# Optimization experiments

Measured on AMD Instinct MI355X. Metric: run time of the kernel, lower is better.

## Reference

```python
import jax, jax.numpy as jnp
import numpy as np

B, S, T = 256, 2048, 64


def setup_inputs() -> dict:
    key = jax.random.key(0)
    k1, k2, k3, k4, k5 = jax.random.split(key, 5)
    emissions = jax.random.normal(k1, (B, S, T), dtype=jnp.float32)
    tags = jax.random.randint(k2, (B, S), 0, T)
    mask = jnp.ones((B, S), dtype=jnp.int32)
    start_transitions = jax.random.uniform(k3, (T,), minval=-1.0, maxval=1.0, dtype=jnp.float32)
    end_transitions = jax.random.uniform(k4, (T,), minval=-1.0, maxval=1.0, dtype=jnp.float32)
    transitions = jax.random.uniform(k5, (T, T), minval=-1.0, maxval=1.0, dtype=jnp.float32)
    return {
        'emissions': emissions,
        'start_transitions': start_transitions,
        'end_transitions': end_transitions,
        'transitions': transitions,
        'tags': tags,
        'mask': mask,
    }


def _crf_nll(emissions, start_transitions, end_transitions, transitions, tags, mask):
    # batch_first=True -> convert to time-major like the torch code
    em = jnp.swapaxes(emissions, 0, 1)            # (S, B, T)
    tg = tags.T                                   # (S, B)
    mk = mask.T.astype(emissions.dtype)           # (S, B)
    barange = jnp.arange(em.shape[1])

    # ---- numerator: score of the gold tag path ----
    score0 = start_transitions[tg[0]] + em[0, barange, tg[0]]  # (B,)

    def num_step(score, inp):
        em_i, tg_prev, tg_i, m_i = inp
        score = score + (transitions[tg_prev, tg_i] + em_i[barange, tg_i]) * m_i
        return score, None

    numerator, _ = jax.lax.scan(num_step, score0, (em[1:], tg[:-1], tg[1:], mk[1:]))
    seq_ends = mk.sum(axis=0).astype(jnp.int32) - 1            # (B,)
    last_tags = tg[seq_ends, barange]
    numerator = numerator + end_transitions[last_tags]

    # ---- denominator: log partition via forward algorithm (log-sum-exp semiring) ----
    alpha0 = start_transitions + em[0]                          # (B, T)

    def den_step(alpha, inp):
        em_i, m_i = inp
        # (B, T_prev, T_next) broadcast-add, reduce over T_prev
        nxt = jax.nn.logsumexp(alpha[:, :, None] + transitions[None, :, :] + em_i[:, None, :], axis=1)
        alpha = jnp.where(m_i[:, None] > 0, nxt, alpha)
        return alpha, None

    alpha, _ = jax.lax.scan(den_step, alpha0, (em[1:], mk[1:]))
    denominator = jax.nn.logsumexp(alpha + end_transitions, axis=1)  # (B,)

    return -(numerator - denominator).mean()


def reference(emissions, start_transitions, end_transitions, transitions, tags, mask):
    return _crf_nll(emissions, start_transitions, end_transitions, transitions, tags, mask)
```

## Files before the change

kernel.cpp:

```cpp
#include <hip/hip_runtime.h>

#define BB 256
#define SS 2048
#define TT 64
#define KC 64
#define LC 32
#define WARM 48
#define NSTEP (WARM + LC)
#define DEN_WAVES (BB * 4)
#define NSLOT 128
#define SLOT_STRIDE 32
#define LN2 0.69314718055994531f
#define LOG2E 1.4426950408889634f

typedef __fp16 half2v __attribute__((ext_vector_type(2)));
typedef __fp16 half8v __attribute__((ext_vector_type(8)));
typedef float float4v __attribute__((ext_vector_type(4)));

__device__ __forceinline__ float4v mfma16(half8v a, half8v b, float4v c) {
  return __builtin_amdgcn_mfma_f32_16x16x32_f16(a, b, c, 0, 0, 0);
}

__global__ __launch_bounds__(64, 1) void crf_kernel(
    const float* __restrict__ em, const float* __restrict__ startT,
    const float* __restrict__ endT, const float* __restrict__ trans,
    const int* __restrict__ tags, const int* __restrict__ mask,
    float* __restrict__ acc, int slotmask) {
  const int lane = threadIdx.x;

  if (blockIdx.x >= DEN_WAVES) {
    const int bb = blockIdx.x - DEN_WAVES;
    const int* tg = tags + bb * SS;
    const int* mp = mask + bb * SS;
    const float* emb = em + (size_t)bb * SS * TT;
    float part = 0.f;
    int cnt = 0;
#pragma unroll 4
    for (int k = 0; k < SS / 64; ++k) {
      int i = k * 64 + lane;
      int m = mp[i];
      cnt += m;
      if (i >= 1 && m) {
        int t1 = tg[i], t0 = tg[i - 1];
        part += trans[t0 * TT + t1] + emb[(size_t)i * TT + t1];
      }
    }
#pragma unroll
    for (int o = 32; o > 0; o >>= 1) {
      part += __shfl_xor(part, o, 64);
      cnt += __shfl_xor(cnt, o, 64);
    }
    if (lane == 0) {
      int t0 = tg[0];
      float num = part + startT[t0] + emb[t0] + endT[tg[cnt - 1]];
      atomicAdd(acc + (size_t)(blockIdx.x & slotmask) * SLOT_STRIDE,
                -num * (1.0f / BB));
    }
    return;
  }

  const int w = blockIdx.x;
  const int L = (w & 7) * (DEN_WAVES / 8) + (w >> 3);
  const int bb = L >> 2;
  const int s = lane & 15;
  const int g = lane >> 4;
  const int c = (L & 3) * 16 + s;
  const float* emB = em + (size_t)bb * SS * TT;
  const size_t rowb = (size_t)bb * SS;

  half8v A[4][2];
#pragma unroll
  for (int mt = 0; mt < 4; ++mt)
#pragma unroll
    for (int kt = 0; kt < 2; ++kt) {
      half8v f;
#pragma unroll
      for (int e = 0; e < 8; e += 2) {
        int k0 = 32 * kt + 16 * (e >> 2) + 4 * g + (e & 3);
        int m = 16 * mt + s;
        float v0 = __expf(trans[k0 * TT + m]) * 0.03125f;
        float v1 = __expf(trans[(k0 + 1) * TT + m]) * 0.03125f;
        half2v p = __builtin_amdgcn_cvt_pkrtz(v0, v1);
        f[e] = p[0];
        f[e + 1] = p[1];
      }
      A[mt][kt] = f;
    }

  half8v B0, B1;
#pragma unroll
  for (int e = 0; e < 8; ++e) {
    B0[e] = (__fp16)0.015625f;
    B1[e] = (__fp16)0.015625f;
  }
  float v_ready = 0.015625f;
  int esum = 0, nsteps = 0;
  float sS = 0.f, gamma = 0.f;
  float4v tf0, tf1, tf2, tf3;

  const int base = c * LC - WARM + 1;

  float4v buf[4][4];

  auto PF = [&](int slot, int idx) {
    int p = base + idx;
    p = p < 0 ? 0 : (p > SS - 1 ? SS - 1 : p);
    const float* r = emB + (size_t)p * TT + 4 * g;
    __builtin_amdgcn_sched_barrier(0);
#pragma unroll
    for (int mt = 0; mt < 4; ++mt) buf[slot][mt] = *(const float4v*)(r + 16 * mt);
    __builtin_amdgcn_sched_barrier(0);
  };
  auto CORE = [&](const float4v (&x)[4]) {
    int eb = __builtin_bit_cast(int, v_ready) & 0x7f800000;
    float sc = __builtin_bit_cast(float, 0x7C000000 - eb);
    esum += eb >> 23;
    nsteps += 1;
    float4v xs0 = x[0] * sc, xs1 = x[1] * sc, xs2 = x[2] * sc, xs3 = x[3] * sc;
    const float4v z = {0.f, 0.f, 0.f, 0.f};
    tf0 = mfma16(A[0][0], B0, z);
    tf0 = mfma16(A[0][1], B1, tf0);
    tf1 = mfma16(A[1][0], B0, z);
    tf1 = mfma16(A[1][1], B1, tf1);
    tf2 = mfma16(A[2][0], B0, z);
    tf2 = mfma16(A[2][1], B1, tf2);
    tf3 = mfma16(A[3][0], B0, z);
    tf3 = mfma16(A[3][1], B1, tf3);
    tf0 *= xs0; tf1 *= xs1; tf2 *= xs2; tf3 *= xs3;
    v_ready = __shfl(tf0[0], s, 64);
    half2v p;
    p = __builtin_amdgcn_cvt_pkrtz(tf0[0], tf0[1]); B0[0] = p[0]; B0[1] = p[1];
    p = __builtin_amdgcn_cvt_pkrtz(tf0[2], tf0[3]); B0[2] = p[0]; B0[3] = p[1];
    p = __builtin_amdgcn_cvt_pkrtz(tf1[0], tf1[1]); B0[4] = p[0]; B0[5] = p[1];
    p = __builtin_amdgcn_cvt_pkrtz(tf1[2], tf1[3]); B0[6] = p[0]; B0[7] = p[1];
    p = __builtin_amdgcn_cvt_pkrtz(tf2[0], tf2[1]); B1[0] = p[0]; B1[1] = p[1];
    p = __builtin_amdgcn_cvt_pkrtz(tf2[2], tf2[3]); B1[2] = p[0]; B1[3] = p[1];
    p = __builtin_amdgcn_cvt_pkrtz(tf3[0], tf3[1]); B1[4] = p[0]; B1[5] = p[1];
    p = __builtin_amdgcn_cvt_pkrtz(tf3[2], tf3[3]); B1[6] = p[0]; B1[7] = p[1];
  };
  auto STEP = [&](int slot, int pfIdx, bool doPf) {
    float4v x[4];
#pragma unroll
    for (int mt = 0; mt < 4; ++mt)
#pragma unroll
      for (int e = 0; e < 4; ++e) x[mt][e] = __expf(buf[slot][mt][e]);
    if (doPf) PF(slot, pfIdx);
    CORE(x);
  };

#pragma unroll
  for (int k = 0; k < 4; ++k) PF(k, k);

  for (int idx = 0; idx < WARM; idx += 4) {
#pragma unroll
    for (int k = 0; k < 4; ++k) STEP(k, idx + k + 4, true);
  }

  {
    float q0b = v_ready;
    sS = __log2f(q0b) + (float)(6 + esum - 116 * nsteps);
    if (c == 0) {
      float aref = startT[0] + emB[0];
      gamma = aref * LOG2E;
      sS = 0.f;
      esum = 0;
      nsteps = 0;
      v_ready = 0.015625f;
#pragma unroll
      for (int e = 0; e < 8; ++e) {
        int t0i = 16 * (e >> 2) + 4 * g + (e & 3);
        B0[e] = (__fp16)(__expf(startT[t0i] + emB[t0i] - aref) * 0.015625f);
        B1[e] = (__fp16)(__expf(startT[t0i + 32] + emB[t0i + 32] - aref) *
                         0.015625f);
      }
    }
  }

  for (int idx = WARM; idx < NSTEP - 4; idx += 4) {
#pragma unroll
    for (int k = 0; k < 4; ++k) STEP(k, idx + k + 4, true);
  }
  STEP(0, 0, false);
  STEP(1, 0, false);
  STEP(2, 0, false);
  float qf;
  {
    half8v oB0 = B0, oB1 = B1;
    float4v o0 = tf0, o1 = tf1, o2 = tf2, o3 = tf3;
    int oes = esum, on = nsteps;
    float ov = v_ready;
    STEP(3, 0, false);
    int p = base + (NSTEP - 1);
    int pc = p > SS - 1 ? SS - 1 : p;
    bool act = (p >= 1) && (p <= SS - 1) && (mask[rowb + pc] != 0);
    qf = act ? v_ready : ov;
    if (!act) {
      B0 = oB0; B1 = oB1; esum = oes; nsteps = on;
      tf0 = o0; tf1 = o1; tf2 = o2; tf3 = o3;
    }
  }

  float eS = __log2f(qf) + (float)(6 + esum - 116 * nsteps) + gamma;
  float contrib = LN2 * (eS - sS);

  {
    float q0l = __log2f(qf);
    float4v ar0, ar1, ar2, ar3;
    float mx = -1e30f;
#pragma unroll
    for (int r = 0; r < 4; ++r) {
      ar0[r] = LN2 * (__log2f(tf0[r]) - q0l) + endT[4 * g + r];
      ar1[r] = LN2 * (__log2f(tf1[r]) - q0l) + endT[16 + 4 * g + r];
      ar2[r] = LN2 * (__log2f(tf2[r]) - q0l) + endT[32 + 4 * g + r];
      ar3[r] = LN2 * (__log2f(tf3[r]) - q0l) + endT[48 + 4 * g + r];
      mx = fmaxf(mx, fmaxf(fmaxf(ar0[r], ar1[r]), fmaxf(ar2[r], ar3[r])));
    }
    mx = fmaxf(mx, __shfl_xor(mx, 16, 64));
    mx = fmaxf(mx, __shfl_xor(mx, 32, 64));
    float ex = 0.f;
#pragma unroll
    for (int r = 0; r < 4; ++r)
      ex += __expf(ar0[r] - mx) + __expf(ar1[r] - mx) + __expf(ar2[r] - mx) +
            __expf(ar3[r] - mx);
    ex += __shfl_xor(ex, 16, 64);
    ex += __shfl_xor(ex, 32, 64);
    if (c == KC - 1) contrib += mx + __logf(ex);
  }

  float val = (g == 0) ? contrib : 0.f;
#pragma unroll
  for (int o = 32; o > 0; o >>= 1) val += __shfl_xor(val, o, 64);
  if (lane == 0)
    atomicAdd(acc + (size_t)(blockIdx.x & slotmask) * SLOT_STRIDE,
              val * (1.0f / BB));
}

__global__ __launch_bounds__(64) void reduce_kernel(const float* __restrict__ ws,
                                                    float* __restrict__ out) {
  float v = ws[(size_t)threadIdx.x * SLOT_STRIDE] +
            ws[(size_t)(threadIdx.x + 64) * SLOT_STRIDE];
#pragma unroll
  for (int o = 32; o > 0; o >>= 1) v += __shfl_xor(v, o, 64);
  if (threadIdx.x == 0) *out = v;
}

extern "C" void kernel_launch(void* const* d_in, const int* in_sizes, int n_in,
                              void* d_out, int out_size, void* d_ws, size_t ws_size,
                              hipStream_t stream) {
  const float* em = (const float*)d_in[0];
  const float* startT = (const float*)d_in[1];
  const float* endT = (const float*)d_in[2];
  const float* trans = (const float*)d_in[3];
  const int* tags = (const int*)d_in[4];
  const int* mask = (const int*)d_in[5];
  float* out = (float*)d_out;

  const size_t need = (size_t)NSLOT * SLOT_STRIDE * sizeof(float);
  if (d_ws && ws_size >= need) {
    (void)hipMemsetAsync(d_ws, 0, need, stream);
    crf_kernel<<<DEN_WAVES + BB, 64, 0, stream>>>(em, startT, endT, trans, tags,
                                                  mask, (float*)d_ws, NSLOT - 1);
    reduce_kernel<<<1, 64, 0, stream>>>((const float*)d_ws, out);
  } else {
    (void)hipMemsetAsync(out, 0, sizeof(float), stream);
    crf_kernel<<<DEN_WAVES + BB, 64, 0, stream>>>(em, startT, endT, trans, tags,
                                                  mask, out, 0);
  }
}
```

Measured before the change: 250.7 us.

## Stream emissions via global_load_lds into an 8-deep LDS ring, shorten warmup

Replaces the 4-slot register prefetch buffer with an 8-slot LDS ring filled by direct global-to-LDS loads, using explicit vmcnt waits to keep several steps of emission rows in flight. This is meant to hide global memory latency in the serial forward recurrence and to free registers. Warmup length also drops from 48 to 32 steps, so each chunk does less redundant work, at the risk of weaker convergence of the warmup approximation. The hand-written vmcnt counts depend on exactly four loads per slot, and the LDS reads rely on no other outstanding memory ops being counted.

```diff
diff --git a/kernel.cpp b/kernel.cpp
--- a/kernel.cpp
+++ b/kernel.cpp
@@ -5,8 +5,9 @@
 #define TT 64
 #define KC 64
 #define LC 32
-#define WARM 48
+#define WARM 32
 #define NSTEP (WARM + LC)
+#define DEPTH 8
 #define DEN_WAVES (BB * 4)
 #define NSLOT 128
 #define SLOT_STRIDE 32
@@ -21,11 +22,14 @@
   return __builtin_amdgcn_mfma_f32_16x16x32_f16(a, b, c, 0, 0, 0);
 }
 
+#define VMW(N) asm volatile("s_waitcnt vmcnt(" #N ")" ::: "memory")
+
 __global__ __launch_bounds__(64, 1) void crf_kernel(
     const float* __restrict__ em, const float* __restrict__ startT,
     const float* __restrict__ endT, const float* __restrict__ trans,
     const int* __restrict__ tags, const int* __restrict__ mask,
     float* __restrict__ acc, int slotmask) {
+  __shared__ float lds[DEPTH * 1024];
   const int lane = threadIdx.x;
 
   if (blockIdx.x >= DEN_WAVES) {
@@ -99,17 +103,28 @@
   float4v tf0, tf1, tf2, tf3;
 
   const int base = c * LC - WARM + 1;
-
-  float4v buf[4][4];
-
-  auto PF = [&](int slot, int idx) {
+  char* lbase = (char*)lds;
+
+  auto PFS = [&](int slot, int idx) {
     int p = base + idx;
     p = p < 0 ? 0 : (p > SS - 1 ? SS - 1 : p);
     const float* r = emB + (size_t)p * TT + 4 * g;
-    __builtin_amdgcn_sched_barrier(0);
-#pragma unroll
-    for (int mt = 0; mt < 4; ++mt) buf[slot][mt] = *(const float4v*)(r + 16 * mt);
-    __builtin_amdgcn_sched_barrier(0);
+    char* d = lbase + slot * 4096;
+#pragma unroll
+    for (int mt = 0; mt < 4; ++mt) {
+      __builtin_amdgcn_global_load_lds(
+          (const __attribute__((address_space(1))) void*)(r + 16 * mt),
+          (__attribute__((address_space(3))) void*)(d + mt * 1024), 16, 0, 0);
+    }
+  };
+  auto LDEXP = [&](int slot, float4v (&x)[4]) {
+    const char* sb = lbase + slot * 4096 + lane * 16;
+#pragma unroll
+    for (int mt = 0; mt < 4; ++mt) x[mt] = *(const float4v*)(sb + mt * 1024);
+#pragma unroll
+    for (int mt = 0; mt < 4; ++mt)
+#pragma unroll
+      for (int e = 0; e < 4; ++e) x[mt][e] = __expf(x[mt][e]);
   };
   auto CORE = [&](const float4v (&x)[4]) {
     int eb = __builtin_bit_cast(int, v_ready) & 0x7f800000;
@@ -138,58 +153,52 @@
     p = __builtin_amdgcn_cvt_pkrtz(tf3[0], tf3[1]); B1[4] = p[0]; B1[5] = p[1];
     p = __builtin_amdgcn_cvt_pkrtz(tf3[2], tf3[3]); B1[6] = p[0]; B1[7] = p[1];
   };
-  auto STEP = [&](int slot, int pfIdx, bool doPf) {
-    float4v x[4];
-#pragma unroll
-    for (int mt = 0; mt < 4; ++mt)
-#pragma unroll
-      for (int e = 0; e < 4; ++e) x[mt][e] = __expf(buf[slot][mt][e]);
-    if (doPf) PF(slot, pfIdx);
-    CORE(x);
-  };
-
-#pragma unroll
-  for (int k = 0; k < 4; ++k) PF(k, k);
-
-  for (int idx = 0; idx < WARM; idx += 4) {
-#pragma unroll
-    for (int k = 0; k < 4; ++k) STEP(k, idx + k + 4, true);
-  }
-
-  {
-    float q0b = v_ready;
-    sS = __log2f(q0b) + (float)(6 + esum - 116 * nsteps);
-    if (c == 0) {
-      float aref = startT[0] + emB[0];
-      gamma = aref * LOG2E;
-      sS = 0.f;
-      esum = 0;
-      nsteps = 0;
-      v_ready = 0.015625f;
-#pragma unroll
-      for (int e = 0; e < 8; ++e) {
-        int t0i = 16 * (e >> 2) + 4 * g + (e & 3);
-        B0[e] = (__fp16)(__expf(startT[t0i] + emB[t0i] - aref) * 0.015625f);
-        B1[e] = (__fp16)(__expf(startT[t0i + 32] + emB[t0i + 32] - aref) *
-                         0.015625f);
+
+#pragma unroll
+  for (int k = 0; k < DEPTH; ++k) PFS(k, k);
+
+  for (int kb = 0; kb < NSTEP - DEPTH; kb += DEPTH) {
+    if (kb == WARM) {
+      sS = __log2f(v_ready) + (float)(6 + esum - 116 * nsteps);
+      if (c == 0) {
+        float aref = startT[0] + emB[0];
+        gamma = aref * LOG2E;
+        sS = 0.f;
+        esum = 0;
+        nsteps = 0;
+        v_ready = 0.015625f;
+#pragma unroll
+        for (int e = 0; e < 8; ++e) {
+          int t0i = 16 * (e >> 2) + 4 * g + (e & 3);
+          B0[e] = (__fp16)(__expf(startT[t0i] + emB[t0i] - aref) * 0.015625f);
+          B1[e] = (__fp16)(__expf(startT[t0i + 32] + emB[t0i + 32] - aref) *
+                           0.015625f);
+        }
       }
     }
-  }
-
-  for (int idx = WARM; idx < NSTEP - 4; idx += 4) {
-#pragma unroll
-    for (int k = 0; k < 4; ++k) STEP(k, idx + k + 4, true);
-  }
-  STEP(0, 0, false);
-  STEP(1, 0, false);
-  STEP(2, 0, false);
+#pragma unroll
+    for (int j = 0; j < DEPTH; ++j) {
+      VMW(28);
+      float4v x[4];
+      LDEXP(j, x);
+      PFS(j, kb + j + DEPTH);
+      CORE(x);
+    }
+  }
+  { VMW(28); float4v x[4]; LDEXP(0, x); CORE(x); }
+  { VMW(24); float4v x[4]; LDEXP(1, x); CORE(x); }
+  { VMW(20); float4v x[4]; LDEXP(2, x); CORE(x); }
+  { VMW(16); float4v x[4]; LDEXP(3, x); CORE(x); }
+  { VMW(12); float4v x[4]; LDEXP(4, x); CORE(x); }
+  { VMW(8);  float4v x[4]; LDEXP(5, x); CORE(x); }
+  { VMW(4);  float4v x[4]; LDEXP(6, x); CORE(x); }
   float qf;
   {
     half8v oB0 = B0, oB1 = B1;
     float4v o0 = tf0, o1 = tf1, o2 = tf2, o3 = tf3;
     int oes = esum, on = nsteps;
     float ov = v_ready;
-    STEP(3, 0, false);
+    { VMW(0); float4v x[4]; LDEXP(7, x); CORE(x); }
     int p = base + (NSTEP - 1);
     int pc = p > SS - 1 ? SS - 1 : p;
     bool act = (p >= 1) && (p <= SS - 1) && (mask[rowb + pc] != 0);
```

Measured after the change: 259.6 us. +3.6%, slower.
